# Performance work log

Measured on AMD Instinct MI355X. Metric: run time of the kernel, lower is better.

Reference implementation:

```python
import jax, jax.numpy as jnp
import numpy as np

D_IN = 256      # input feature size
D_OUT = 64      # per-head output size (forced by fc=Linear(64,1) and out buffer)
HEADS = 8
B = 32768
N = 4           # nodes per graph (hardcoded in original forward)
LRELU_ALPHA = 0.2
NEG_INF = -9.0e15


def setup_inputs() -> dict:
    key = jax.random.key(0)
    ks = jax.random.split(key, 8)

    def xavier(k, shape, gain=1.414):
        fan_in, fan_out = shape[0], shape[1]
        limit = gain * np.sqrt(6.0 / (fan_in + fan_out))
        return jax.random.uniform(k, shape, jnp.float32, -limit, limit)

    x = jax.random.normal(ks[0], (B, N, D_IN), jnp.float32)
    adj = jax.random.normal(ks[1], (B, N, N), jnp.float32)  # mask via adj > 0
    W = xavier(ks[2], (D_IN, D_OUT))
    a = xavier(ks[3], (2 * D_OUT, 1))
    W2 = xavier(ks[4], (D_OUT * HEADS, D_OUT))
    a2 = xavier(ks[5], (2 * D_OUT, 1))
    fc_w = jax.random.normal(ks[6], (1, D_OUT), jnp.float32) * (1.0 / np.sqrt(D_OUT))
    fc_b = jnp.zeros((1,), jnp.float32)
    return {"x": x, "adj": adj, "W": W, "a": a, "W2": W2, "a2": a2,
            "fc_w": fc_w, "fc_b": fc_b}


def _gal(h, adj, Wp, ap, concat):
    # h: [B,N,Din], Wp: [Din,Dout], ap: [2*Dout,1]
    Wh = jnp.einsum('bni,io->bno', h, Wp)            # [B,N,Dout]
    f_src = Wh @ ap[:D_OUT]                          # [B,N,1]
    f_dst = Wh @ ap[D_OUT:]                          # [B,N,1]
    e = jax.nn.leaky_relu(f_src + jnp.swapaxes(f_dst, 1, 2), LRELU_ALPHA)  # [B,N,N]
    e = jnp.where(adj > 0, e, NEG_INF)
    att = jax.nn.softmax(e, axis=-1)                 # torch softmax(dim=1) on 2D == last axis
    hp = jnp.einsum('bnm,bmo->bno', att, Wh)         # [B,N,Dout]
    return jax.nn.elu(hp) if concat else hp


def reference(x, adj, W, a, W2, a2, fc_w, fc_b):
    h1 = _gal(x, adj, W, a, concat=True)             # [B,N,64]
    # all heads share the same module object -> concat == tile of one head
    hcat = jnp.tile(h1, (1, 1, HEADS))               # [B,N,512]
    out = _gal(hcat, adj, W2, a2, concat=False)      # [B,N,64]
    out = out[:, 0, :]                               # [B,64]
    return out @ fc_w.T + fc_b                       # [B,1]
```

## Files before the change

### kernel.cpp

```cpp
#include <hip/hip_runtime.h>
#include <hip/hip_bf16.h>
#include <stdint.h>

#define LRELU_ALPHA 0.2f
#define NEG_INF -9000000000000000.0f
#define NB 32768
#define NTASKS (NB/16)

typedef float f32x4 __attribute__((ext_vector_type(4)));
typedef short s16x8 __attribute__((ext_vector_type(8)));

__device__ __forceinline__ unsigned short f2bf(float f){
  unsigned int u = __float_as_uint(f);
  u += 0x7fffu + ((u >> 16) & 1u);
  return (unsigned short)(u >> 16);
}

__global__ void prep_kernel(const float* __restrict__ W, const float* __restrict__ W2,
                            unsigned short* __restrict__ wsp){
  int t = blockIdx.x * blockDim.x + threadIdx.x;
  if (t < 64*256){
    int o = t & 63, k = t >> 6;
    wsp[o*256 + (k ^ ((o & 7) << 3))] = f2bf(W[k*64 + o]);
  }
  if (t < 64*64){
    int o = t & 63, c = t >> 6;
    float s = 0.f;
    #pragma unroll
    for (int h = 0; h < 8; ++h) s += W2[(h*64 + c)*64 + o];
    wsp[16384 + o*64 + (c ^ ((o & 7) << 3))] = f2bf(s);
  }
}

__launch_bounds__(256, 3)
__global__ void gat_kernel(const float* __restrict__ x, const float* __restrict__ adj,
                           const float* __restrict__ a, const float* __restrict__ a2,
                           const float* __restrict__ fc_w, const float* __restrict__ fc_b,
                           const unsigned short* __restrict__ wsp,
                           float* __restrict__ out){
  __shared__ __align__(16) unsigned short smem[24576];
  const int tid = threadIdx.x;
  {
    const uint4* src = (const uint4*)wsp;
    uint4* dst = (uint4*)smem;
    #pragma unroll
    for (int i = 0; i < 10; ++i) dst[tid + 256*i] = src[tid + 256*i];
  }
  __syncthreads();

  const int p  = tid & 15;
  const int g  = (tid >> 4) & 3;
  const int wv = tid >> 6;
  const int lbase = tid & 48;

  float aS[4], aD[4], a2S[4], a2D[4], fw[4];
  #pragma unroll
  for (int ct = 0; ct < 4; ++ct){
    aS[ct]  = a[ct*16 + p];
    aD[ct]  = a[64 + ct*16 + p];
    a2S[ct] = a2[ct*16 + p];
    a2D[ct] = a2[64 + ct*16 + p];
    fw[ct]  = fc_w[ct*16 + p];
  }
  const float fcb = fc_b[0];
  const int hbase = 20480 + wv*1024;

  for (int it = blockIdx.x; it < NTASKS; it += gridDim.x){
    const int b0 = it*16 + wv*4;
    const float adjv = adj[(size_t)(b0 + g)*16 + p];

    f32x4 acc[4];
    #pragma unroll
    for (int ct = 0; ct < 4; ++ct) acc[ct] = (f32x4){0.f,0.f,0.f,0.f};
    const float* xrow = x + ((size_t)(b0 + (p >> 2))*4 + (p & 3))*256 + g*8;
    #pragma unroll
    for (int kk = 0; kk < 8; ++kk){
      float4 f0 = *(const float4*)(xrow + kk*32);
      float4 f1 = *(const float4*)(xrow + kk*32 + 4);
      union { s16x8 v; unsigned short u[8]; } af;
      af.u[0]=f2bf(f0.x); af.u[1]=f2bf(f0.y); af.u[2]=f2bf(f0.z); af.u[3]=f2bf(f0.w);
      af.u[4]=f2bf(f1.x); af.u[5]=f2bf(f1.y); af.u[6]=f2bf(f1.z); af.u[7]=f2bf(f1.w);
      const int kb = kk*32 + g*8;
      #pragma unroll
      for (int ct = 0; ct < 4; ++ct){
        const int o = ct*16 + p;
        s16x8 bf = *(const s16x8*)&smem[o*256 + (kb ^ ((o & 7) << 3))];
        acc[ct] = __builtin_amdgcn_mfma_f32_16x16x32_bf16(af.v, bf, acc[ct], 0, 0, 0);
      }
    }

    float fs[4], fd[4];
    #pragma unroll
    for (int r = 0; r < 4; ++r){
      float s1 = 0.f, s2 = 0.f;
      #pragma unroll
      for (int ct = 0; ct < 4; ++ct){ s1 += acc[ct][r]*aS[ct]; s2 += acc[ct][r]*aD[ct]; }
      fs[r] = s1; fd[r] = s2;
    }
    #pragma unroll
    for (int msk = 1; msk < 16; msk <<= 1){
      #pragma unroll
      for (int r = 0; r < 4; ++r){
        fs[r] += __shfl_xor(fs[r], msk);
        fd[r] += __shfl_xor(fd[r], msk);
      }
    }
    float fsi = (p & 8) ? ((p & 4) ? fs[3] : fs[2]) : ((p & 4) ? fs[1] : fs[0]);
    float fdj = (p & 2) ? ((p & 1) ? fd[3] : fd[2]) : ((p & 1) ? fd[1] : fd[0]);
    float ev = fsi + fdj;
    ev = (ev > 0.f) ? ev : LRELU_ALPHA*ev;
    ev = (adjv > 0.f) ? ev : NEG_INF;
    float mx = fmaxf(ev, __shfl_xor(ev, 1));
    mx = fmaxf(mx, __shfl_xor(mx, 2));
    float pe = __expf(ev - mx);
    float se = pe + __shfl_xor(pe, 1);
    se += __shfl_xor(se, 2);
    const float att = pe / se;

    #pragma unroll
    for (int r = 0; r < 4; ++r){
      float b0a = __shfl(att, lbase + r*4 + 0);
      float b1a = __shfl(att, lbase + r*4 + 1);
      float b2a = __shfl(att, lbase + r*4 + 2);
      float b3a = __shfl(att, lbase + r*4 + 3);
      const int mr = g*4 + r;
      #pragma unroll
      for (int ct = 0; ct < 4; ++ct){
        float hp = b0a*acc[ct][0] + b1a*acc[ct][1] + b2a*acc[ct][2] + b3a*acc[ct][3];
        hp = (hp > 0.f) ? hp : expm1f(hp);
        const int c = ct*16 + p;
        smem[hbase + mr*64 + (c ^ ((mr & 7) << 3))] = f2bf(hp);
      }
    }
    asm volatile("" ::: "memory");

    f32x4 acc2[4];
    #pragma unroll
    for (int ct = 0; ct < 4; ++ct) acc2[ct] = (f32x4){0.f,0.f,0.f,0.f};
    #pragma unroll
    for (int kk = 0; kk < 2; ++kk){
      const int kb = kk*32 + g*8;
      s16x8 a2f = *(const s16x8*)&smem[hbase + p*64 + (kb ^ ((p & 7) << 3))];
      #pragma unroll
      for (int ct = 0; ct < 4; ++ct){
        const int o = ct*16 + p;
        s16x8 b2f = *(const s16x8*)&smem[16384 + o*64 + (kb ^ ((o & 7) << 3))];
        acc2[ct] = __builtin_amdgcn_mfma_f32_16x16x32_bf16(a2f, b2f, acc2[ct], 0, 0, 0);
      }
    }

    float fd2[4], sv[4], fs20 = 0.f;
    #pragma unroll
    for (int r = 0; r < 4; ++r){
      float s1 = 0.f, s2 = 0.f;
      #pragma unroll
      for (int ct = 0; ct < 4; ++ct){ s1 += acc2[ct][r]*a2D[ct]; s2 += acc2[ct][r]*fw[ct]; }
      fd2[r] = s1; sv[r] = s2;
    }
    #pragma unroll
    for (int ct = 0; ct < 4; ++ct) fs20 += acc2[ct][0]*a2S[ct];
    #pragma unroll
    for (int msk = 1; msk < 16; msk <<= 1){
      #pragma unroll
      for (int r = 0; r < 4; ++r){
        fd2[r] += __shfl_xor(fd2[r], msk);
        sv[r]  += __shfl_xor(sv[r],  msk);
      }
      fs20 += __shfl_xor(fs20, msk);
    }
    float e2[4];
    #pragma unroll
    for (int j = 0; j < 4; ++j){
      float adj0 = __shfl(adjv, lbase + j);
      float tv = fs20 + fd2[j];
      tv = (tv > 0.f) ? tv : LRELU_ALPHA*tv;
      e2[j] = (adj0 > 0.f) ? tv : NEG_INF;
    }
    float m2 = fmaxf(fmaxf(e2[0], e2[1]), fmaxf(e2[2], e2[3]));
    float s2s = 0.f, ov = 0.f;
    #pragma unroll
    for (int j = 0; j < 4; ++j){
      float pj = __expf(e2[j] - m2);
      s2s += pj; ov += pj*sv[j];
    }
    if (p == 0) out[b0 + g] = ov/s2s + fcb;
  }
}

extern "C" void kernel_launch(void* const* d_in, const int* in_sizes, int n_in,
                              void* d_out, int out_size, void* d_ws, size_t ws_size,
                              hipStream_t stream){
  (void)in_sizes; (void)n_in; (void)out_size; (void)ws_size;
  const float* x   = (const float*)d_in[0];
  const float* adj = (const float*)d_in[1];
  const float* W   = (const float*)d_in[2];
  const float* a   = (const float*)d_in[3];
  const float* W2  = (const float*)d_in[4];
  const float* a2  = (const float*)d_in[5];
  const float* fcw = (const float*)d_in[6];
  const float* fcb = (const float*)d_in[7];
  float* out = (float*)d_out;
  unsigned short* wsp = (unsigned short*)d_ws;

  hipLaunchKernelGGL(prep_kernel, dim3(64), dim3(256), 0, stream, W, W2, wsp);
  hipLaunchKernelGGL(gat_kernel, dim3(1024), dim3(256), 0, stream,
                     x, adj, a, a2, fcw, fcb, wsp, out);
}
```

Baseline: 46.48 us.

## Prefetch next task's x and adj into registers, trim grid, use fast expm1

The persistent loop now loads the next iteration's 16 float4 of x and its adj value into registers right after the first MFMA stage, so the global loads overlap with the attention and second-layer compute. The grid drops from 1024 to 768 blocks, likely to fit one wave of resident blocks. The bf16 conversion uses the packed __float22bfloat162_rn intrinsic and ELU uses __expf-1 instead of expm1f. In exchange it adds 32 VGPRs of prefetch buffer per thread, which may hurt occupancy under launch_bounds(256,3), and the fast ELU loses a little accuracy near zero.

```diff
diff --git a/kernel.cpp b/kernel.cpp
--- a/kernel.cpp
+++ b/kernel.cpp
@@ -6,6 +6,7 @@
 #define NEG_INF -9000000000000000.0f
 #define NB 32768
 #define NTASKS (NB/16)
+#define GRID 768
 
 typedef float f32x4 __attribute__((ext_vector_type(4)));
 typedef short s16x8 __attribute__((ext_vector_type(8)));
@@ -65,27 +66,55 @@
   const float fcb = fc_b[0];
   const int hbase = 20480 + wv*1024;
 
-  for (int it = blockIdx.x; it < NTASKS; it += gridDim.x){
+  float4 xb[8][2];
+  float adv;
+  {
+    const int b0 = blockIdx.x*16 + wv*4;
+    const float* xrow = x + ((size_t)(b0 + (p >> 2))*4 + (p & 3))*256 + g*8;
+    #pragma unroll
+    for (int kk = 0; kk < 8; ++kk){
+      xb[kk][0] = *(const float4*)(xrow + kk*32);
+      xb[kk][1] = *(const float4*)(xrow + kk*32 + 4);
+    }
+    adv = adj[(size_t)(b0 + g)*16 + p];
+  }
+
+  for (int it = blockIdx.x; it < NTASKS; it += GRID){
     const int b0 = it*16 + wv*4;
-    const float adjv = adj[(size_t)(b0 + g)*16 + p];
+    const float adjv = adv;
 
     f32x4 acc[4];
     #pragma unroll
     for (int ct = 0; ct < 4; ++ct) acc[ct] = (f32x4){0.f,0.f,0.f,0.f};
-    const float* xrow = x + ((size_t)(b0 + (p >> 2))*4 + (p & 3))*256 + g*8;
     #pragma unroll
     for (int kk = 0; kk < 8; ++kk){
-      float4 f0 = *(const float4*)(xrow + kk*32);
-      float4 f1 = *(const float4*)(xrow + kk*32 + 4);
-      union { s16x8 v; unsigned short u[8]; } af;
-      af.u[0]=f2bf(f0.x); af.u[1]=f2bf(f0.y); af.u[2]=f2bf(f0.z); af.u[3]=f2bf(f0.w);
-      af.u[4]=f2bf(f1.x); af.u[5]=f2bf(f1.y); af.u[6]=f2bf(f1.z); af.u[7]=f2bf(f1.w);
+      float4 f0 = xb[kk][0];
+      float4 f1 = xb[kk][1];
+      union { s16x8 v; __hip_bfloat162 h2[4]; } af;
+      af.h2[0] = __float22bfloat162_rn(make_float2(f0.x, f0.y));
+      af.h2[1] = __float22bfloat162_rn(make_float2(f0.z, f0.w));
+      af.h2[2] = __float22bfloat162_rn(make_float2(f1.x, f1.y));
+      af.h2[3] = __float22bfloat162_rn(make_float2(f1.z, f1.w));
       const int kb = kk*32 + g*8;
       #pragma unroll
       for (int ct = 0; ct < 4; ++ct){
         const int o = ct*16 + p;
         s16x8 bf = *(const s16x8*)&smem[o*256 + (kb ^ ((o & 7) << 3))];
         acc[ct] = __builtin_amdgcn_mfma_f32_16x16x32_bf16(af.v, bf, acc[ct], 0, 0, 0);
+      }
+    }
+
+    {
+      const int itn = it + GRID;
+      if (itn < NTASKS){
+        const int b0n = itn*16 + wv*4;
+        const float* xrow = x + ((size_t)(b0n + (p >> 2))*4 + (p & 3))*256 + g*8;
+        #pragma unroll
+        for (int kk = 0; kk < 8; ++kk){
+          xb[kk][0] = *(const float4*)(xrow + kk*32);
+          xb[kk][1] = *(const float4*)(xrow + kk*32 + 4);
+        }
+        adv = adj[(size_t)(b0n + g)*16 + p];
       }
     }
 
@@ -127,7 +156,7 @@
       #pragma unroll
       for (int ct = 0; ct < 4; ++ct){
         float hp = b0a*acc[ct][0] + b1a*acc[ct][1] + b2a*acc[ct][2] + b3a*acc[ct][3];
-        hp = (hp > 0.f) ? hp : expm1f(hp);
+        hp = (hp > 0.f) ? hp : (__expf(hp) - 1.0f);
         const int c = ct*16 + p;
         smem[hbase + mr*64 + (c ^ ((mr & 7) << 3))] = f2bf(hp);
       }
@@ -203,6 +232,6 @@
   unsigned short* wsp = (unsigned short*)d_ws;
 
   hipLaunchKernelGGL(prep_kernel, dim3(64), dim3(256), 0, stream, W, W2, wsp);
-  hipLaunchKernelGGL(gat_kernel, dim3(1024), dim3(256), 0, stream,
+  hipLaunchKernelGGL(gat_kernel, dim3(GRID), dim3(256), 0, stream,
                      x, adj, a, a2, fcw, fcb, wsp, out);
 }
```

After: 38.49 us. 17.2% less time.
